# Performance work log

Measured on AMD Instinct MI355X. Metric: run time of the kernel, lower is better.

The kernel has to match this reference:

```python
import jax, jax.numpy as jnp
import numpy as np

N_NODES = 100_000
N_EDGES = 1_600_000
NODE_FEATURES = 22


def setup_inputs() -> dict:
    key = jax.random.key(0)
    ks = jax.random.split(key, 10)
    s = 0.1
    x = jax.random.normal(ks[0], (N_NODES, NODE_FEATURES), dtype=jnp.float32)
    edge_index = jax.random.randint(ks[1], (2, N_EDGES), 0, N_NODES, dtype=jnp.int64)
    return {
        "x": x,
        "edge_index": edge_index,
        "W_embed": jax.random.normal(ks[2], (NODE_FEATURES, 32), jnp.float32) * s,
        "b_embed": jax.random.normal(ks[3], (32,), jnp.float32) * s,
        "W1": jax.random.normal(ks[4], (32, 32), jnp.float32) * s,
        "b1": jax.random.normal(ks[5], (32,), jnp.float32) * s,
        "W2": jax.random.normal(ks[6], (64, 32), jnp.float32) * s,
        "b2": jax.random.normal(ks[7], (32,), jnp.float32) * s,
        "W_pred": jax.random.normal(ks[8], (64, 1), jnp.float32) * s,
        "b_pred": jax.random.normal(ks[9], (1,), jnp.float32) * s,
    }


def gcn_conv(h, src, dst, deg_inv_sqrt, W, b, num_nodes):
    """PyG GCNConv: h' = scatter_add(norm_ij * (h W)[src] -> dst) + b.
    src/dst already include self-loops; deg_inv_sqrt precomputed on dst."""
    h = h @ W  # [N, out]
    norm = deg_inv_sqrt[src] * deg_inv_sqrt[dst]  # [E]
    msg = h[src] * norm[:, None]  # gather + normalize
    out = jax.ops.segment_sum(msg, dst, num_segments=num_nodes)  # scatter-add
    return out + b


def reference(x, edge_index, W_embed, b_embed, W1, b1, W2, b2, W_pred, b_pred):
    n = x.shape[0]
    loop = jnp.arange(n, dtype=edge_index.dtype)
    src = jnp.concatenate([edge_index[0], loop])  # add self-loops
    dst = jnp.concatenate([edge_index[1], loop])
    deg = jax.ops.segment_sum(jnp.ones_like(src, dtype=x.dtype), dst, num_segments=n)
    deg_inv_sqrt = jnp.where(deg > 0, jax.lax.rsqrt(jnp.maximum(deg, 1.0)), 0.0)

    h = x @ W_embed + b_embed  # MLP_embed
    # dropout is identity at eval time
    h0 = h
    h = gcn_conv(h, src, dst, deg_inv_sqrt, W1, b1, n)
    h = jax.nn.relu(h)
    h = jnp.concatenate([h, h0], axis=1)  # [N, 64]
    h = gcn_conv(h, src, dst, deg_inv_sqrt, W2, b2, n)
    h = jax.nn.relu(h)
    h = jnp.concatenate([h, h0], axis=1)  # [N, 64]
    delta = h @ W_pred + b_pred  # [N, 1]
    out = jax.nn.relu(delta + x[:, 1:2])
    return out
```

## Files before the change

### kernel.cpp

```cpp
#include <hip/hip_runtime.h>
#include <hip/hip_bf16.h>

#define NF 22
#define H  32
#define BSH 8
#define CAP 8192
#define CHUNK 2048

__device__ __forceinline__ float bflo(unsigned int v) { return __uint_as_float(v << 16); }
__device__ __forceinline__ float bfhi(unsigned int v) { return __uint_as_float(v & 0xffff0000u); }

__global__ void init_cur(int* __restrict__ cursor, int NB) {
    int i = blockIdx.x * blockDim.x + threadIdx.x;
    if (i < NB) cursor[i] = i * CAP;
}

__global__ __launch_bounds__(256) void bin_edges(
    const int* __restrict__ src, const int* __restrict__ dst,
    int* __restrict__ cursor, int* __restrict__ binned, int E, int NB)
{
    __shared__ int lh[512];
    __shared__ int lcur[512];
    int tid = threadIdx.x;
    for (int j = tid; j < NB; j += 256) lh[j] = 0;
    __syncthreads();
    int e0 = blockIdx.x * CHUNK;
    int ee = min(e0 + CHUNK, E);
    for (int i = e0 + tid; i < ee; i += 256) atomicAdd(&lh[dst[i] >> BSH], 1);
    __syncthreads();
    for (int j = tid; j < NB; j += 256) {
        int c = lh[j];
        if (c) lcur[j] = atomicAdd(&cursor[j], c);
    }
    __syncthreads();
    for (int i = e0 + tid; i < ee; i += 256) {
        int d = dst[i];
        int p = atomicAdd(&lcur[d >> BSH], 1);
        binned[p] = (src[i] << BSH) | (d & 255);
    }
}

__global__ __launch_bounds__(1024) void bucket_csr(
    const int* __restrict__ cursor, const int* __restrict__ binned,
    int* __restrict__ rowptr, int* __restrict__ rowcnt, int* __restrict__ sorted_src,
    float* __restrict__ dis, int N)
{
    __shared__ int cnt[256];
    __shared__ int s[256];
    __shared__ int lcur[256];
    int b = blockIdx.x, tid = threadIdx.x;
    int bn = b << BSH;
    if (tid < 256) cnt[tid] = 0;
    __syncthreads();
    int es = b * CAP, ee = cursor[b];
    for (int i = es + tid; i < ee; i += 1024) atomicAdd(&cnt[binned[i] & 255], 1);
    __syncthreads();
    int v = 0;
    if (tid < 256) { v = cnt[tid]; s[tid] = v; }
    __syncthreads();
    for (int off = 1; off < 256; off <<= 1) {
        int t = 0;
        if (tid < 256 && tid >= off) t = s[tid - off];
        __syncthreads();
        if (tid < 256) s[tid] += t;
        __syncthreads();
    }
    if (tid < 256) {
        int ex = s[tid] - v;
        lcur[tid] = ex;
        int n = bn + tid;
        if (n < N) {
            rowptr[n] = es + ex;
            rowcnt[n] = v;
            dis[n] = rsqrtf((float)(v + 1));
        }
    }
    __syncthreads();
    for (int i = es + tid; i < ee; i += 1024) {
        int e = binned[i];
        int p = atomicAdd(&lcur[e & 255], 1);
        sorted_src[es + p] = e >> BSH;
    }
}

__global__ __launch_bounds__(256) void embed_g1(
    const float* __restrict__ x, const float* __restrict__ We,
    const float* __restrict__ be, const float* __restrict__ W1,
    const float* __restrict__ W2, const float* __restrict__ Wp,
    const float* __restrict__ bp, const float* __restrict__ dis,
    __hip_bfloat16* __restrict__ g, __hip_bfloat16* __restrict__ y2,
    float* __restrict__ hp, int N)
{
    __shared__ float sWe[NF * H];
    __shared__ float sW1[H * H];
    __shared__ float sW2b[H * H];
    __shared__ float sbe[H];
    __shared__ float sWpb[H];
    __shared__ float sx[8][NF];
    __shared__ float sh[8][H];

    int tid = threadIdx.x;
    for (int j = tid; j < NF * H; j += 256) sWe[j] = We[j];
    for (int j = tid; j < H * H; j += 256) sW1[j] = W1[j];
    for (int j = tid; j < H * H; j += 256) sW2b[j] = W2[H * H + j];
    if (tid < H) sbe[tid] = be[tid];
    if (tid >= H && tid < 2 * H) sWpb[tid - H] = Wp[tid];

    int grp = tid >> 5, t = tid & 31;
    int node = blockIdx.x * 8 + grp;
    int nodec = node < N ? node : N - 1;
    if (t < NF) sx[grp][t] = x[(size_t)nodec * NF + t];
    __syncthreads();

    float h = sbe[t];
#pragma unroll
    for (int k = 0; k < NF; k++) h += sx[grp][k] * sWe[k * H + t];
    sh[grp][t] = h;
    __syncthreads();

    float di = dis[nodec];
    float gv = 0.f, yv = 0.f;
#pragma unroll
    for (int k = 0; k < H; k++) {
        float hv = sh[grp][k];
        gv += hv * sW1[k * H + t];
        yv += hv * sW2b[k * H + t];
    }
    gv *= di;

    float pv = h * sWpb[t];
#pragma unroll
    for (int off = 16; off > 0; off >>= 1) pv += __shfl_down(pv, off, 32);

    if (node < N) {
        size_t o = (size_t)node * H + t;
        g[o] = __float2bfloat16(gv);
        y2[o] = __float2bfloat16(yv);
        if (t == 0) hp[node] = pv + bp[0] + sx[grp][1];
    }
}

__global__ __launch_bounds__(256) void agg_mid(
    const int* __restrict__ rowptr, const int* __restrict__ rowcnt,
    const int* __restrict__ sorted_src,
    const __hip_bfloat16* __restrict__ g_in, const __hip_bfloat16* __restrict__ y2,
    const float* __restrict__ dis, const float* __restrict__ W2,
    const float* __restrict__ b1, __hip_bfloat16* __restrict__ g_out, int N)
{
    __shared__ float sW2[H * H];
    __shared__ float srow[16][33];

    int tid = threadIdx.x;
    for (int j = tid; j < H * H; j += 256) sW2[j] = W2[j];

    int grp = tid >> 4, lane = tid & 15;
    int node = blockIdx.x * 16 + grp;
    int nodec = node < N ? node : N - 1;

    const unsigned int* gv = (const unsigned int*)g_in;
    unsigned int sv = gv[(size_t)nodec * 16 + lane];
    float ax = bflo(sv), ay = bfhi(sv);

    int start = rowptr[nodec];
    int end = start + rowcnt[nodec];
    int i = start;
    for (; i + 7 < end; i += 8) {
        int s0 = sorted_src[i],     s1 = sorted_src[i + 1];
        int s2 = sorted_src[i + 2], s3 = sorted_src[i + 3];
        int s4 = sorted_src[i + 4], s5 = sorted_src[i + 5];
        int s6 = sorted_src[i + 6], s7 = sorted_src[i + 7];
        unsigned int v0 = gv[(size_t)s0 * 16 + lane], v1 = gv[(size_t)s1 * 16 + lane];
        unsigned int v2 = gv[(size_t)s2 * 16 + lane], v3 = gv[(size_t)s3 * 16 + lane];
        unsigned int v4 = gv[(size_t)s4 * 16 + lane], v5 = gv[(size_t)s5 * 16 + lane];
        unsigned int v6 = gv[(size_t)s6 * 16 + lane], v7 = gv[(size_t)s7 * 16 + lane];
        ax += bflo(v0) + bflo(v1) + bflo(v2) + bflo(v3)
            + bflo(v4) + bflo(v5) + bflo(v6) + bflo(v7);
        ay += bfhi(v0) + bfhi(v1) + bfhi(v2) + bfhi(v3)
            + bfhi(v4) + bfhi(v5) + bfhi(v6) + bfhi(v7);
    }
    for (; i + 3 < end; i += 4) {
        int s0 = sorted_src[i],     s1 = sorted_src[i + 1];
        int s2 = sorted_src[i + 2], s3 = sorted_src[i + 3];
        unsigned int v0 = gv[(size_t)s0 * 16 + lane], v1 = gv[(size_t)s1 * 16 + lane];
        unsigned int v2 = gv[(size_t)s2 * 16 + lane], v3 = gv[(size_t)s3 * 16 + lane];
        ax += bflo(v0) + bflo(v1) + bflo(v2) + bflo(v3);
        ay += bfhi(v0) + bfhi(v1) + bfhi(v2) + bfhi(v3);
    }
    for (; i < end; i++) {
        unsigned int v = gv[(size_t)sorted_src[i] * 16 + lane];
        ax += bflo(v); ay += bfhi(v);
    }

    float di = dis[nodec];
    float2 bb = ((const float2*)b1)[lane];
    srow[grp][2 * lane]     = fmaxf(di * ax + bb.x, 0.f);
    srow[grp][2 * lane + 1] = fmaxf(di * ay + bb.y, 0.f);
    __syncthreads();

    const float2* sW2v = (const float2*)sW2;
    float o0 = 0.f, o1 = 0.f;
#pragma unroll
    for (int k = 0; k < H; k++) {
        float rv = srow[grp][k];
        float2 w = sW2v[k * 16 + lane];
        o0 += rv * w.x;
        o1 += rv * w.y;
    }
    unsigned int yv = ((const unsigned int*)y2)[(size_t)nodec * 16 + lane];
    o0 = di * (o0 + bflo(yv));
    o1 = di * (o1 + bfhi(yv));

    if (node < N) {
        __hip_bfloat162 p;
        p.x = __float2bfloat16(o0);
        p.y = __float2bfloat16(o1);
        ((__hip_bfloat162*)g_out)[(size_t)node * 16 + lane] = p;
    }
}

__global__ __launch_bounds__(256) void agg_final(
    const int* __restrict__ rowptr, const int* __restrict__ rowcnt,
    const int* __restrict__ sorted_src,
    const __hip_bfloat16* __restrict__ g_in, const float* __restrict__ hp,
    const float* __restrict__ dis, const float* __restrict__ b2,
    const float* __restrict__ Wp, float* __restrict__ out, int N)
{
    int gid = blockIdx.x * blockDim.x + threadIdx.x;
    int node = gid >> 4;
    if (node >= N) return;
    int lane = gid & 15;

    const unsigned int* gv = (const unsigned int*)g_in;
    unsigned int sv = gv[(size_t)node * 16 + lane];
    float ax = bflo(sv), ay = bfhi(sv);

    int start = rowptr[node];
    int end = start + rowcnt[node];
    int i = start;
    for (; i + 7 < end; i += 8) {
        int s0 = sorted_src[i],     s1 = sorted_src[i + 1];
        int s2 = sorted_src[i + 2], s3 = sorted_src[i + 3];
        int s4 = sorted_src[i + 4], s5 = sorted_src[i + 5];
        int s6 = sorted_src[i + 6], s7 = sorted_src[i + 7];
        unsigned int v0 = gv[(size_t)s0 * 16 + lane], v1 = gv[(size_t)s1 * 16 + lane];
        unsigned int v2 = gv[(size_t)s2 * 16 + lane], v3 = gv[(size_t)s3 * 16 + lane];
        unsigned int v4 = gv[(size_t)s4 * 16 + lane], v5 = gv[(size_t)s5 * 16 + lane];
        unsigned int v6 = gv[(size_t)s6 * 16 + lane], v7 = gv[(size_t)s7 * 16 + lane];
        ax += bflo(v0) + bflo(v1) + bflo(v2) + bflo(v3)
            + bflo(v4) + bflo(v5) + bflo(v6) + bflo(v7);
        ay += bfhi(v0) + bfhi(v1) + bfhi(v2) + bfhi(v3)
            + bfhi(v4) + bfhi(v5) + bfhi(v6) + bfhi(v7);
    }
    for (; i + 3 < end; i += 4) {
        int s0 = sorted_src[i],     s1 = sorted_src[i + 1];
        int s2 = sorted_src[i + 2], s3 = sorted_src[i + 3];
        unsigned int v0 = gv[(size_t)s0 * 16 + lane], v1 = gv[(size_t)s1 * 16 + lane];
        unsigned int v2 = gv[(size_t)s2 * 16 + lane], v3 = gv[(size_t)s3 * 16 + lane];
        ax += bflo(v0) + bflo(v1) + bflo(v2) + bflo(v3);
        ay += bfhi(v0) + bfhi(v1) + bfhi(v2) + bfhi(v3);
    }
    for (; i < end; i++) {
        unsigned int v = gv[(size_t)sorted_src[i] * 16 + lane];
        ax += bflo(v); ay += bfhi(v);
    }

    float di = dis[node];
    float2 b2v = ((const float2*)b2)[lane];
    float2 wpa = ((const float2*)Wp)[lane];
    float v = fmaxf(di * ax + b2v.x, 0.f) * wpa.x
            + fmaxf(di * ay + b2v.y, 0.f) * wpa.y;
#pragma unroll
    for (int off = 8; off > 0; off >>= 1) v += __shfl_down(v, off, 16);
    if (lane == 0) out[node] = fmaxf(v + hp[node], 0.f);
}

extern "C" void kernel_launch(void* const* d_in, const int* in_sizes, int n_in,
                              void* d_out, int out_size, void* d_ws, size_t ws_size,
                              hipStream_t stream) {
    const float* x  = (const float*)d_in[0];
    const int*   ei = (const int*)d_in[1];
    const float* We = (const float*)d_in[2];
    const float* be = (const float*)d_in[3];
    const float* W1 = (const float*)d_in[4];
    const float* b1 = (const float*)d_in[5];
    const float* W2 = (const float*)d_in[6];
    const float* b2 = (const float*)d_in[7];
    const float* Wp = (const float*)d_in[8];
    const float* bp = (const float*)d_in[9];
    float* out = (float*)d_out;

    const int N = in_sizes[0] / NF;
    const int E = in_sizes[1] / 2;
    const int* src = ei;
    const int* dst = ei + E;
    const int NB = (N + 255) >> BSH;
    const int nchunk = (E + CHUNK - 1) / CHUNK;

    size_t Np  = ((size_t)N + 127) & ~(size_t)127;
    size_t NHp = ((size_t)N * H + 127) & ~(size_t)127;
    float* ws  = (float*)d_ws;
    float* dis = ws;
    float* hp  = dis + Np;
    __hip_bfloat16* g1 = (__hip_bfloat16*)(hp + Np);
    __hip_bfloat16* g2 = g1 + NHp;
    __hip_bfloat16* y2 = g2 + NHp;
    int* cursor     = (int*)(y2 + NHp);
    int* rowptr     = cursor + 512;
    int* rowcnt     = rowptr + Np;
    int* binned     = rowcnt + Np;
    int* sorted_src = binned + (size_t)NB * CAP;

    init_cur<<<2, 256, 0, stream>>>(cursor, NB);
    bin_edges<<<nchunk, 256, 0, stream>>>(src, dst, cursor, binned, E, NB);
    bucket_csr<<<NB, 1024, 0, stream>>>(cursor, binned, rowptr, rowcnt, sorted_src, dis, N);

    embed_g1<<<(N + 7) / 8, 256, 0, stream>>>(x, We, be, W1, W2, Wp, bp, dis, g1, y2, hp, N);
    agg_mid<<<(N + 15) / 16, 256, 0, stream>>>(rowptr, rowcnt, sorted_src, g1, y2, dis, W2, b1, g2, N);
    agg_final<<<((size_t)N * 16 + 255) / 256, 256, 0, stream>>>(rowptr, rowcnt, sorted_src, g2, hp, dis, b2, Wp, out, N);
}
```

Measured before the change: 223.6 us.

## Widen gather to 8-byte loads with 8 lanes per node; persist embed blocks

The aggregation kernels now assign 8 lanes per node instead of 16, and each lane gathers a uint2 (four bf16 values). This halves the number of gather instructions and doubles the nodes handled per wave, and the mid-layer matvec switches to float4 weight reads. The embed kernel becomes grid-stride with at most 1536 blocks, so the shared-memory weight loads are amortised over many node groups. The trade-offs are fewer threads in flight for hiding gather latency and extra barriers inside the embed loop.

Result: faster. 217.6 us (-2.7%).

```diff
diff --git a/kernel.cpp b/kernel.cpp
--- a/kernel.cpp
+++ b/kernel.cpp
@@ -9,6 +9,10 @@
 
 __device__ __forceinline__ float bflo(unsigned int v) { return __uint_as_float(v << 16); }
 __device__ __forceinline__ float bfhi(unsigned int v) { return __uint_as_float(v & 0xffff0000u); }
+__device__ __forceinline__ unsigned int packbf2(float a, float b) {
+    __hip_bfloat162 p; p.x = __float2bfloat16(a); p.y = __float2bfloat16(b);
+    return *(unsigned int*)&p;
+}
 
 __global__ void init_cur(int* __restrict__ cursor, int NB) {
     int i = blockIdx.x * blockDim.x + threadIdx.x;
@@ -107,36 +111,40 @@
     if (tid >= H && tid < 2 * H) sWpb[tid - H] = Wp[tid];
 
     int grp = tid >> 5, t = tid & 31;
-    int node = blockIdx.x * 8 + grp;
-    int nodec = node < N ? node : N - 1;
-    if (t < NF) sx[grp][t] = x[(size_t)nodec * NF + t];
-    __syncthreads();
-
-    float h = sbe[t];
-#pragma unroll
-    for (int k = 0; k < NF; k++) h += sx[grp][k] * sWe[k * H + t];
-    sh[grp][t] = h;
-    __syncthreads();
-
-    float di = dis[nodec];
-    float gv = 0.f, yv = 0.f;
-#pragma unroll
-    for (int k = 0; k < H; k++) {
-        float hv = sh[grp][k];
-        gv += hv * sW1[k * H + t];
-        yv += hv * sW2b[k * H + t];
-    }
-    gv *= di;
-
-    float pv = h * sWpb[t];
-#pragma unroll
-    for (int off = 16; off > 0; off >>= 1) pv += __shfl_down(pv, off, 32);
-
-    if (node < N) {
-        size_t o = (size_t)node * H + t;
-        g[o] = __float2bfloat16(gv);
-        y2[o] = __float2bfloat16(yv);
-        if (t == 0) hp[node] = pv + bp[0] + sx[grp][1];
+    int ngrp = (N + 7) >> 3;
+    for (int nb = blockIdx.x; nb < ngrp; nb += gridDim.x) {
+        int node = nb * 8 + grp;
+        int nodec = node < N ? node : N - 1;
+        __syncthreads();
+        if (t < NF) sx[grp][t] = x[(size_t)nodec * NF + t];
+        __syncthreads();
+
+        float h = sbe[t];
+#pragma unroll
+        for (int k = 0; k < NF; k++) h += sx[grp][k] * sWe[k * H + t];
+        sh[grp][t] = h;
+        __syncthreads();
+
+        float di = dis[nodec];
+        float gv = 0.f, yv = 0.f;
+#pragma unroll
+        for (int k = 0; k < H; k++) {
+            float hv = sh[grp][k];
+            gv += hv * sW1[k * H + t];
+            yv += hv * sW2b[k * H + t];
+        }
+        gv *= di;
+
+        float pv = h * sWpb[t];
+#pragma unroll
+        for (int off = 16; off > 0; off >>= 1) pv += __shfl_down(pv, off, 32);
+
+        if (node < N) {
+            size_t o = (size_t)node * H + t;
+            g[o] = __float2bfloat16(gv);
+            y2[o] = __float2bfloat16(yv);
+            if (t == 0) hp[node] = pv + bp[0] + sx[grp][1];
+        }
     }
 }
 
@@ -148,18 +156,18 @@
     const float* __restrict__ b1, __hip_bfloat16* __restrict__ g_out, int N)
 {
     __shared__ float sW2[H * H];
-    __shared__ float srow[16][33];
+    __shared__ float srow[32][33];
 
     int tid = threadIdx.x;
     for (int j = tid; j < H * H; j += 256) sW2[j] = W2[j];
 
-    int grp = tid >> 4, lane = tid & 15;
-    int node = blockIdx.x * 16 + grp;
+    int grp = tid >> 3, lane = tid & 7;
+    int node = blockIdx.x * 32 + grp;
     int nodec = node < N ? node : N - 1;
 
-    const unsigned int* gv = (const unsigned int*)g_in;
-    unsigned int sv = gv[(size_t)nodec * 16 + lane];
-    float ax = bflo(sv), ay = bfhi(sv);
+    const uint2* gv2 = (const uint2*)g_in;
+    uint2 sv = gv2[(size_t)nodec * 8 + lane];
+    float a0 = bflo(sv.x), a1 = bfhi(sv.x), a2 = bflo(sv.y), a3 = bfhi(sv.y);
 
     int start = rowptr[nodec];
     int end = start + rowcnt[nodec];
@@ -169,52 +177,51 @@
         int s2 = sorted_src[i + 2], s3 = sorted_src[i + 3];
         int s4 = sorted_src[i + 4], s5 = sorted_src[i + 5];
         int s6 = sorted_src[i + 6], s7 = sorted_src[i + 7];
-        unsigned int v0 = gv[(size_t)s0 * 16 + lane], v1 = gv[(size_t)s1 * 16 + lane];
-        unsigned int v2 = gv[(size_t)s2 * 16 + lane], v3 = gv[(size_t)s3 * 16 + lane];
-        unsigned int v4 = gv[(size_t)s4 * 16 + lane], v5 = gv[(size_t)s5 * 16 + lane];
-        unsigned int v6 = gv[(size_t)s6 * 16 + lane], v7 = gv[(size_t)s7 * 16 + lane];
-        ax += bflo(v0) + bflo(v1) + bflo(v2) + bflo(v3)
-            + bflo(v4) + bflo(v5) + bflo(v6) + bflo(v7);
-        ay += bfhi(v0) + bfhi(v1) + bfhi(v2) + bfhi(v3)
-            + bfhi(v4) + bfhi(v5) + bfhi(v6) + bfhi(v7);
-    }
-    for (; i + 3 < end; i += 4) {
-        int s0 = sorted_src[i],     s1 = sorted_src[i + 1];
-        int s2 = sorted_src[i + 2], s3 = sorted_src[i + 3];
-        unsigned int v0 = gv[(size_t)s0 * 16 + lane], v1 = gv[(size_t)s1 * 16 + lane];
-        unsigned int v2 = gv[(size_t)s2 * 16 + lane], v3 = gv[(size_t)s3 * 16 + lane];
-        ax += bflo(v0) + bflo(v1) + bflo(v2) + bflo(v3);
-        ay += bfhi(v0) + bfhi(v1) + bfhi(v2) + bfhi(v3);
+        uint2 v0 = gv2[(size_t)s0 * 8 + lane], v1 = gv2[(size_t)s1 * 8 + lane];
+        uint2 v2 = gv2[(size_t)s2 * 8 + lane], v3 = gv2[(size_t)s3 * 8 + lane];
+        uint2 v4 = gv2[(size_t)s4 * 8 + lane], v5 = gv2[(size_t)s5 * 8 + lane];
+        uint2 v6 = gv2[(size_t)s6 * 8 + lane], v7 = gv2[(size_t)s7 * 8 + lane];
+        a0 += bflo(v0.x) + bflo(v1.x) + bflo(v2.x) + bflo(v3.x)
+            + bflo(v4.x) + bflo(v5.x) + bflo(v6.x) + bflo(v7.x);
+        a1 += bfhi(v0.x) + bfhi(v1.x) + bfhi(v2.x) + bfhi(v3.x)
+            + bfhi(v4.x) + bfhi(v5.x) + bfhi(v6.x) + bfhi(v7.x);
+        a2 += bflo(v0.y) + bflo(v1.y) + bflo(v2.y) + bflo(v3.y)
+            + bflo(v4.y) + bflo(v5.y) + bflo(v6.y) + bflo(v7.y);
+        a3 += bfhi(v0.y) + bfhi(v1.y) + bfhi(v2.y) + bfhi(v3.y)
+            + bfhi(v4.y) + bfhi(v5.y) + bfhi(v6.y) + bfhi(v7.y);
     }
     for (; i < end; i++) {
-        unsigned int v = gv[(size_t)sorted_src[i] * 16 + lane];
-        ax += bflo(v); ay += bfhi(v);
+        uint2 v = gv2[(size_t)sorted_src[i] * 8 + lane];
+        a0 += bflo(v.x); a1 += bfhi(v.x); a2 += bflo(v.y); a3 += bfhi(v.y);
     }
 
     float di = dis[nodec];
-    float2 bb = ((const float2*)b1)[lane];
-    srow[grp][2 * lane]     = fmaxf(di * ax + bb.x, 0.f);
-    srow[grp][2 * lane + 1] = fmaxf(di * ay + bb.y, 0.f);
-    __syncthreads();
-
-    const float2* sW2v = (const float2*)sW2;
-    float o0 = 0.f, o1 = 0.f;
+    float4 bb = ((const float4*)b1)[lane];
+    srow[grp][4 * lane]     = fmaxf(di * a0 + bb.x, 0.f);
+    srow[grp][4 * lane + 1] = fmaxf(di * a1 + bb.y, 0.f);
+    srow[grp][4 * lane + 2] = fmaxf(di * a2 + bb.z, 0.f);
+    srow[grp][4 * lane + 3] = fmaxf(di * a3 + bb.w, 0.f);
+    __syncthreads();
+
+    const float4* sW2v = (const float4*)sW2;
+    float o0 = 0.f, o1 = 0.f, o2 = 0.f, o3 = 0.f;
 #pragma unroll
     for (int k = 0; k < H; k++) {
         float rv = srow[grp][k];
-        float2 w = sW2v[k * 16 + lane];
-        o0 += rv * w.x;
-        o1 += rv * w.y;
-    }
-    unsigned int yv = ((const unsigned int*)y2)[(size_t)nodec * 16 + lane];
-    o0 = di * (o0 + bflo(yv));
-    o1 = di * (o1 + bfhi(yv));
+        float4 w = sW2v[k * 8 + lane];
+        o0 += rv * w.x; o1 += rv * w.y; o2 += rv * w.z; o3 += rv * w.w;
+    }
+    uint2 yv = ((const uint2*)y2)[(size_t)nodec * 8 + lane];
+    o0 = di * (o0 + bflo(yv.x));
+    o1 = di * (o1 + bfhi(yv.x));
+    o2 = di * (o2 + bflo(yv.y));
+    o3 = di * (o3 + bfhi(yv.y));
 
     if (node < N) {
-        __hip_bfloat162 p;
-        p.x = __float2bfloat16(o0);
-        p.y = __float2bfloat16(o1);
-        ((__hip_bfloat162*)g_out)[(size_t)node * 16 + lane] = p;
+        uint2 p;
+        p.x = packbf2(o0, o1);
+        p.y = packbf2(o2, o3);
+        ((uint2*)g_out)[(size_t)node * 8 + lane] = p;
     }
 }
 
@@ -226,13 +233,13 @@
     const float* __restrict__ Wp, float* __restrict__ out, int N)
 {
     int gid = blockIdx.x * blockDim.x + threadIdx.x;
-    int node = gid >> 4;
+    int node = gid >> 3;
     if (node >= N) return;
-    int lane = gid & 15;
-
-    const unsigned int* gv = (const unsigned int*)g_in;
-    unsigned int sv = gv[(size_t)node * 16 + lane];
-    float ax = bflo(sv), ay = bfhi(sv);
+    int lane = gid & 7;
+
+    const uint2* gv2 = (const uint2*)g_in;
+    uint2 sv = gv2[(size_t)node * 8 + lane];
+    float a0 = bflo(sv.x), a1 = bfhi(sv.x), a2 = bflo(sv.y), a3 = bfhi(sv.y);
 
     int start = rowptr[node];
     int end = start + rowcnt[node];
@@ -242,35 +249,33 @@
         int s2 = sorted_src[i + 2], s3 = sorted_src[i + 3];
         int s4 = sorted_src[i + 4], s5 = sorted_src[i + 5];
         int s6 = sorted_src[i + 6], s7 = sorted_src[i + 7];
-        unsigned int v0 = gv[(size_t)s0 * 16 + lane], v1 = gv[(size_t)s1 * 16 + lane];
-        unsigned int v2 = gv[(size_t)s2 * 16 + lane], v3 = gv[(size_t)s3 * 16 + lane];
-        unsigned int v4 = gv[(size_t)s4 * 16 + lane], v5 = gv[(size_t)s5 * 16 + lane];
-        unsigned int v6 = gv[(size_t)s6 * 16 + lane], v7 = gv[(size_t)s7 * 16 + lane];
-        ax += bflo(v0) + bflo(v1) + bflo(v2) + bflo(v3)
-            + bflo(v4) + bflo(v5) + bflo(v6) + bflo(v7);
-        ay += bfhi(v0) + bfhi(v1) + bfhi(v2) + bfhi(v3)
-            + bfhi(v4) + bfhi(v5) + bfhi(v6) + bfhi(v7);
-    }
-    for (; i + 3 < end; i += 4) {
-        int s0 = sorted_src[i],     s1 = sorted_src[i + 1];
-        int s2 = sorted_src[i + 2], s3 = sorted_src[i + 3];
-        unsigned int v0 = gv[(size_t)s0 * 16 + lane], v1 = gv[(size_t)s1 * 16 + lane];
-        unsigned int v2 = gv[(size_t)s2 * 16 + lane], v3 = gv[(size_t)s3 * 16 + lane];
-        ax += bflo(v0) + bflo(v1) + bflo(v2) + bflo(v3);
-        ay += bfhi(v0) + bfhi(v1) + bfhi(v2) + bfhi(v3);
+        uint2 v0 = gv2[(size_t)s0 * 8 + lane], v1 = gv2[(size_t)s1 * 8 + lane];
+        uint2 v2 = gv2[(size_t)s2 * 8 + lane], v3 = gv2[(size_t)s3 * 8 + lane];
+        uint2 v4 = gv2[(size_t)s4 * 8 + lane], v5 = gv2[(size_t)s5 * 8 + lane];
+        uint2 v6 = gv2[(size_t)s6 * 8 + lane], v7 = gv2[(size_t)s7 * 8 + lane];
+        a0 += bflo(v0.x) + bflo(v1.x) + bflo(v2.x) + bflo(v3.x)
+            + bflo(v4.x) + bflo(v5.x) + bflo(v6.x) + bflo(v7.x);
+        a1 += bfhi(v0.x) + bfhi(v1.x) + bfhi(v2.x) + bfhi(v3.x)
+            + bfhi(v4.x) + bfhi(v5.x) + bfhi(v6.x) + bfhi(v7.x);
+        a2 += bflo(v0.y) + bflo(v1.y) + bflo(v2.y) + bflo(v3.y)
+            + bflo(v4.y) + bflo(v5.y) + bflo(v6.y) + bflo(v7.y);
+        a3 += bfhi(v0.y) + bfhi(v1.y) + bfhi(v2.y) + bfhi(v3.y)
+            + bfhi(v4.y) + bfhi(v5.y) + bfhi(v6.y) + bfhi(v7.y);
     }
     for (; i < end; i++) {
-        unsigned int v = gv[(size_t)sorted_src[i] * 16 + lane];
-        ax += bflo(v); ay += bfhi(v);
+        uint2 v = gv2[(size_t)sorted_src[i] * 8 + lane];
+        a0 += bflo(v.x); a1 += bfhi(v.x); a2 += bflo(v.y); a3 += bfhi(v.y);
     }
 
     float di = dis[node];
-    float2 b2v = ((const float2*)b2)[lane];
-    float2 wpa = ((const float2*)Wp)[lane];
-    float v = fmaxf(di * ax + b2v.x, 0.f) * wpa.x
-            + fmaxf(di * ay + b2v.y, 0.f) * wpa.y;
-#pragma unroll
-    for (int off = 8; off > 0; off >>= 1) v += __shfl_down(v, off, 16);
+    float4 b2v = ((const float4*)b2)[lane];
+    float4 wp  = ((const float4*)Wp)[lane];
+    float v = fmaxf(di * a0 + b2v.x, 0.f) * wp.x
+            + fmaxf(di * a1 + b2v.y, 0.f) * wp.y
+            + fmaxf(di * a2 + b2v.z, 0.f) * wp.z
+            + fmaxf(di * a3 + b2v.w, 0.f) * wp.w;
+#pragma unroll
+    for (int off = 4; off > 0; off >>= 1) v += __shfl_down(v, off, 8);
     if (lane == 0) out[node] = fmaxf(v + hp[node], 0.f);
 }
 
@@ -314,7 +319,9 @@
     bin_edges<<<nchunk, 256, 0, stream>>>(src, dst, cursor, binned, E, NB);
     bucket_csr<<<NB, 1024, 0, stream>>>(cursor, binned, rowptr, rowcnt, sorted_src, dis, N);
 
-    embed_g1<<<(N + 7) / 8, 256, 0, stream>>>(x, We, be, W1, W2, Wp, bp, dis, g1, y2, hp, N);
-    agg_mid<<<(N + 15) / 16, 256, 0, stream>>>(rowptr, rowcnt, sorted_src, g1, y2, dis, W2, b1, g2, N);
-    agg_final<<<((size_t)N * 16 + 255) / 256, 256, 0, stream>>>(rowptr, rowcnt, sorted_src, g2, hp, dis, b2, Wp, out, N);
-}
+    int ngrp = (N + 7) >> 3;
+    int eg = ngrp < 1536 ? ngrp : 1536;
+    embed_g1<<<eg, 256, 0, stream>>>(x, We, be, W1, W2, Wp, bp, dis, g1, y2, hp, N);
+    agg_mid<<<(N + 31) / 32, 256, 0, stream>>>(rowptr, rowcnt, sorted_src, g1, y2, dis, W2, b1, g2, N);
+    agg_final<<<((size_t)N * 8 + 255) / 256, 256, 0, stream>>>(rowptr, rowcnt, sorted_src, g2, hp, dis, b2, Wp, out, N);
+}
```
